# Kernel tuning notes

Hardware: AMD Instinct MI355X
Metric: run time of the kernel (lower is better)

The kernel has to match this reference:

```python
import jax, jax.numpy as jnp
import numpy as np

B = 131072
GI, GO = 4, 4          # input/output pathway groups
NI, NO = 64, 32        # neurons per input group (256/4), per output group (128/4)


def _gelu(t):
    # torch F.gelu default = exact erf gelu
    return jax.nn.gelu(t, approximate=False)


def setup_inputs() -> dict:
    key = jax.random.key(0)
    ks = jax.random.split(key, 16)
    s = 0.02
    return {
        "x":  jax.random.normal(ks[0], (B, 784), jnp.float32),
        "W1": jax.random.normal(ks[1], (512, 784), jnp.float32) * s,
        "b1": jax.random.normal(ks[2], (512,), jnp.float32) * s,
        "W2": jax.random.normal(ks[3], (256, 512), jnp.float32) * s,
        "b2": jax.random.normal(ks[4], (256,), jnp.float32) * s,
        "W3": jax.random.normal(ks[5], (128, 256), jnp.float32) * s,
        "b3": jax.random.normal(ks[6], (128,), jnp.float32) * s,
        "W4": jax.random.normal(ks[7], (64, 128), jnp.float32) * s,
        "b4": jax.random.normal(ks[8], (64,), jnp.float32) * s,
        "W5": jax.random.normal(ks[9], (32, 64), jnp.float32) * s,
        "b5": jax.random.normal(ks[10], (32,), jnp.float32) * s,
        "W6": jax.random.normal(ks[11], (10, 32), jnp.float32) * s,
        "b6": jax.random.normal(ks[12], (10,), jnp.float32) * s,
        "Wr": jax.random.normal(ks[13], (GI * GO, 256), jnp.float32) * s,
        "br": jax.random.normal(ks[14], (GI * GO,), jnp.float32) * s,
    }


def reference(x, W1, b1, W2, b2, W3, b3, W4, b4, W5, b5, W6, b6, Wr, br):
    # pre-middle dense chain (middle_layer == 3)
    h = _gelu(x @ W1.T + b1)          # [B, 512]
    mid_in = _gelu(h @ W2.T + b2)     # [B, 256]

    # router over 16 pathways; pathway_idx = i*GO + j -> reshape [B, GI, GO]
    pw = jax.nn.softmax(mid_in @ Wr.T + br, axis=-1).reshape(-1, GI, GO)

    # grouped pathway matmuls on fc3 (contiguous neuron groups -> reshape)
    xi = mid_in.reshape(-1, GI, NI)            # [B, GI, NI]
    W3g = W3.reshape(GO, NO, GI, NI)           # [GO, NO, GI, NI]
    part = jnp.einsum('bgi,ongi->bgon', xi, W3g)            # [B, GI, GO, NO]
    part = part + b3.reshape(GO, NO)[None, None]            # bias per pathway
    mid_out = jnp.einsum('bgo,bgon->bon', pw, part).reshape(-1, GO * NO)  # [B,128]
    mid_out = _gelu(mid_out)

    # post-middle dense chain
    h = _gelu(mid_out @ W4.T + b4)    # [B, 64]
    h = _gelu(h @ W5.T + b5)          # [B, 32]
    return h @ W6.T + b6              # [B, 10]
```

## Files before the change

kernel.cpp:

```cpp
#include <hip/hip_runtime.h>
#include <cstdint>

typedef _Float16 f16;
typedef _Float16 f16x4 __attribute__((ext_vector_type(4)));
typedef _Float16 f16x8 __attribute__((ext_vector_type(8)));
typedef float f32x4 __attribute__((ext_vector_type(4)));

#define MFMA16(a, b, c) __builtin_amdgcn_mfma_f32_16x16x32_f16((a), (b), (c), 0, 0, 0)
#define SBAR() __builtin_amdgcn_s_barrier()
#define SCHEDB() __builtin_amdgcn_sched_barrier(0)

__device__ __forceinline__ float gelu_f(float x) {
    const float u = x * (1.5957691216f + 0.0713548163f * x * x);
    return x * __builtin_amdgcn_rcpf(1.0f + __expf(-u));
}

__device__ __forceinline__ void load_lds16(const void* g, void* l) {
    __builtin_amdgcn_global_load_lds(
        (const __attribute__((address_space(1))) void*)(uintptr_t)g,
        (__attribute__((address_space(3))) void*)(uint32_t)(uintptr_t)l,
        16, 0, 0);
}

__global__ void k_prep(const float* __restrict__ W1, const float* __restrict__ W2,
                       const float* __restrict__ W3, const float* __restrict__ W4,
                       const float* __restrict__ W5, const float* __restrict__ W6,
                       const float* __restrict__ Wr,
                       f16* __restrict__ W1p, f16* __restrict__ W2f, f16* __restrict__ W3f,
                       f16* __restrict__ W4f, f16* __restrict__ W5f, f16* __restrict__ W6p,
                       f16* __restrict__ Wrf) {
    int i = blockIdx.x * 256 + threadIdx.x;
    if (i < 425984) {
        int r = i / 832, c = i - r * 832;
        W1p[i] = (f16)(c < 784 ? W1[r * 784 + c] : 0.0f);
        return;
    }
    i -= 425984;
    if (i < 131072) { W2f[i] = (f16)W2[i]; return; }
    i -= 131072;
    if (i < 32768) { W3f[i] = (f16)W3[i]; return; }
    i -= 32768;
    if (i < 8192) { W4f[i] = (f16)W4[i]; return; }
    i -= 8192;
    if (i < 2048) { W5f[i] = (f16)W5[i]; return; }
    i -= 2048;
    if (i < 512) {
        int r = i >> 5, c = i & 31;
        W6p[i] = (f16)(r < 10 ? W6[r * 32 + c] : 0.0f);
        return;
    }
    i -= 512;
    if (i < 4096) { Wrf[i] = (f16)Wr[i]; return; }
}

__global__ __launch_bounds__(256, 2)
void k_gemm1(const float* __restrict__ A, const f16* __restrict__ Bw,
             const float* __restrict__ bias, f16* __restrict__ C) {
    __shared__ float As[2][128 * 32];
    __shared__ f16   Bs[2][256 * 32];
    const int tid = threadIdx.x;
    const int wave = tid >> 6, lane = tid & 63;
    const int nt = blockIdx.x & 1;
    const size_t mt = blockIdx.x >> 1;
    const size_t row0 = mt * 128;
    const int col0 = nt * 256;
    const int am = lane & 15, akg = lane >> 4;
    const int wm = (wave & 1) * 64, wn = (wave >> 1) * 128;
    const f32x4 zero4 = {0.f, 0.f, 0.f, 0.f};
    f32x4 acc[4][8];
#pragma unroll
    for (int i = 0; i < 4; ++i)
#pragma unroll
        for (int j = 0; j < 8; ++j) acc[i][j] = zero4;

    const int arow_l = lane >> 3, aps = lane & 7;
    const int brow_l = lane >> 2, bps = lane & 3;

    auto stage = [&](int kt, int buf) {
        const int kb = kt * 32;
#pragma unroll
        for (int i = 0; i < 4; ++i) {
            const int inst = wave * 4 + i;
            const int row = inst * 8 + arow_l;
            const int ls = aps ^ (row & 7);
            int c = kb + ls * 4;
            if (c > 780) c = 768;
            load_lds16(A + (row0 + row) * (size_t)784 + c, &As[buf][inst * 256]);
        }
#pragma unroll
        for (int i = 0; i < 4; ++i) {
            const int inst = wave * 4 + i;
            const int row = inst * 16 + brow_l;
            const int ls = bps ^ ((row >> 1) & 3);
            load_lds16(Bw + (size_t)(col0 + row) * 832 + kb + ls * 8, &Bs[buf][inst * 512]);
        }
    };

    stage(0, 0);

    for (int kt = 0; kt < 26; ++kt) {
        const int cur = kt & 1;
        if (kt + 1 < 26) {
            stage(kt + 1, cur ^ 1);
            asm volatile("s_waitcnt vmcnt(8)" ::: "memory");
        } else {
            asm volatile("s_waitcnt vmcnt(0)" ::: "memory");
        }
        SBAR();
        SCHEDB();
        f16x8 af[4];
#pragma unroll
        for (int i = 0; i < 4; ++i) {
            const int row = wm + i * 16 + am;
            const int rx = row & 7;
            const f32x4 lo = *(const f32x4*)&As[cur][row * 32 + (((akg << 1) ^ rx) << 2)];
            const f32x4 hi = *(const f32x4*)&As[cur][row * 32 + ((((akg << 1) | 1) ^ rx) << 2)];
            f16x8 v;
            v[0] = (f16)lo[0]; v[1] = (f16)lo[1]; v[2] = (f16)lo[2]; v[3] = (f16)lo[3];
            v[4] = (f16)hi[0]; v[5] = (f16)hi[1]; v[6] = (f16)hi[2]; v[7] = (f16)hi[3];
            af[i] = v;
        }
        f16x8 bf[8];
#pragma unroll
        for (int j = 0; j < 8; ++j) {
            const int row = wn + j * 16 + am;
            bf[j] = *(const f16x8*)&Bs[cur][row * 32 + ((akg ^ ((row >> 1) & 3)) << 3)];
        }
#pragma unroll
        for (int i = 0; i < 4; ++i)
#pragma unroll
            for (int j = 0; j < 8; ++j)
                acc[i][j] = MFMA16(bf[j], af[i], acc[i][j]);
        SCHEDB();
        if (kt + 1 < 26) SBAR();
    }
    const int cc = akg * 4;
#pragma unroll
    for (int i = 0; i < 4; ++i) {
        const size_t row = row0 + wm + i * 16 + am;
#pragma unroll
        for (int j = 0; j < 8; ++j) {
            const int col = col0 + wn + j * 16 + cc;
            const float4 b4 = *(const float4*)(bias + col);
            f16x4 v;
            v[0] = (f16)gelu_f(acc[i][j][0] + b4.x);
            v[1] = (f16)gelu_f(acc[i][j][1] + b4.y);
            v[2] = (f16)gelu_f(acc[i][j][2] + b4.z);
            v[3] = (f16)gelu_f(acc[i][j][3] + b4.w);
            *(f16x4*)(C + row * 512 + col) = v;
        }
    }
}

__global__ __launch_bounds__(512, 2)
void k_mid(const f16* __restrict__ H1v, const f16* __restrict__ W2f,
           const float* __restrict__ b2,
           const f16* __restrict__ W3f, const float* __restrict__ b3,
           const f16* __restrict__ W4f, const float* __restrict__ b4,
           const f16* __restrict__ W5f, const float* __restrict__ b5,
           const f16* __restrict__ W6p, const float* __restrict__ b6v,
           const f16* __restrict__ Wrf, const float* __restrict__ brv,
           float* __restrict__ OUT) {
    __shared__ __align__(16) char smem[141312];
    f16* Am = (f16*)smem;
    f16* Bm = (f16*)(smem + 32768);
    f16* s_mid = (f16*)smem;
    float* s_pw = (float*)(smem + 67584);
    f16* s_mo = (f16*)(smem + 77824);
    f16* s_h4 = (f16*)(smem + 112640);
    f16* s_h5 = (f16*)(smem + 131072);
    const int tid = threadIdx.x, wave = tid >> 6, lane = tid & 63;
    const size_t row0 = (size_t)blockIdx.x * 128;
    const int am = lane & 15, akg = lane >> 4, ak = akg * 8;
    const int wm = (wave & 1) * 64, wn = (wave >> 1) * 64;
    const f32x4 zero4 = {0.f, 0.f, 0.f, 0.f};
    f32x4 acc[4][4];
#pragma unroll
    for (int i = 0; i < 4; ++i)
#pragma unroll
        for (int j = 0; j < 4; ++j) acc[i][j] = zero4;

    auto stage = [&](int kt, int buf) {
        const int kb = kt * 64;
#pragma unroll
        for (int t = 0; t < 2; ++t) {
            const int idx = t * 512 + tid;
            const int row = idx >> 3;
            const int ls = (idx & 7) ^ (row & 7);
            load_lds16(H1v + (row0 + row) * 512 + kb + ls * 8,
                       Am + buf * 8192 + (t * 512 + wave * 64) * 8);
        }
#pragma unroll
        for (int t = 0; t < 4; ++t) {
            const int idx = t * 512 + tid;
            const int row = idx >> 3;
            const int ls = (idx & 7) ^ (row & 7);
            load_lds16(W2f + (size_t)row * 512 + kb + ls * 8,
                       Bm + buf * 16384 + (t * 512 + wave * 64) * 8);
        }
    };

    stage(0, 0);
    for (int kt = 0; kt < 8; ++kt) {
        const int cur = kt & 1;
        if (kt + 1 < 8) {
            stage(kt + 1, cur ^ 1);
            asm volatile("s_waitcnt vmcnt(6)" ::: "memory");
        } else {
            asm volatile("s_waitcnt vmcnt(0)" ::: "memory");
        }
        SBAR();
        SCHEDB();
#pragma unroll
        for (int ks = 0; ks < 2; ++ks) {
            f16x8 af[4], bf[4];
#pragma unroll
            for (int i = 0; i < 4; ++i) {
                const int row = wm + i * 16 + am;
                af[i] = *(const f16x8*)&Am[cur * 8192 + row * 64 +
                                           ((((ks << 2) | akg) ^ (row & 7)) << 3)];
            }
#pragma unroll
            for (int j = 0; j < 4; ++j) {
                const int row = wn + j * 16 + am;
                bf[j] = *(const f16x8*)&Bm[cur * 16384 + row * 64 +
                                           ((((ks << 2) | akg) ^ (row & 7)) << 3)];
            }
#pragma unroll
            for (int i = 0; i < 4; ++i)
#pragma unroll
                for (int j = 0; j < 4; ++j)
                    acc[i][j] = MFMA16(bf[j], af[i], acc[i][j]);
        }
        SCHEDB();
        asm volatile("s_waitcnt lgkmcnt(0)" ::: "memory");
        SBAR();
    }
    {
        const int cc = akg * 4;
#pragma unroll
        for (int i = 0; i < 4; ++i) {
            const int row = wm + i * 16 + am;
#pragma unroll
            for (int j = 0; j < 4; ++j) {
                const int col = wn + j * 16 + cc;
                const float4 bb = *(const float4*)(b2 + col);
                f16x4 v;
                v[0] = (f16)gelu_f(acc[i][j][0] + bb.x);
                v[1] = (f16)gelu_f(acc[i][j][1] + bb.y);
                v[2] = (f16)gelu_f(acc[i][j][2] + bb.z);
                v[3] = (f16)gelu_f(acc[i][j][3] + bb.w);
                *(f16x4*)&s_mid[row * 264 + col] = v;
            }
        }
    }
    __syncthreads();

    const int wr = wave * 16;
    const int crow = wr + akg * 4;

    {
        f32x4 lacc = zero4;
#pragma unroll
        for (int ks = 0; ks < 8; ++ks) {
            f16x8 a = *(const f16x8*)(s_mid + (wr + am) * 264 + ks * 32 + ak);
            f16x8 b = *(const f16x8*)(Wrf + am * 256 + ks * 32 + ak);
            lacc = MFMA16(a, b, lacc);
        }
        const float brn = brv[am];
#pragma unroll
        for (int r = 0; r < 4; ++r) {
            float l = lacc[r] + brn;
            float mx = l;
#pragma unroll
            for (int m = 1; m <= 8; m <<= 1) mx = fmaxf(mx, __shfl_xor(mx, m));
            const float e = __expf(l - mx);
            float s = e;
#pragma unroll
            for (int m = 1; m <= 8; m <<= 1) s += __shfl_xor(s, m);
            const float p = e / s;
            float sg = p;
            sg += __shfl_xor(sg, 4);
            sg += __shfl_xor(sg, 8);
            s_pw[(crow + r) * 20 + am] = p;
            if (am < 4) s_pw[(crow + r) * 20 + 16 + am] = sg;
        }
    }

    {
        f16x8 a3[4][2];
#pragma unroll
        for (int g = 0; g < 4; ++g)
#pragma unroll
            for (int kh = 0; kh < 2; ++kh)
                a3[g][kh] = *(const f16x8*)(s_mid + (wr + am) * 264 + g * 64 + kh * 32 + ak);
#pragma unroll
        for (int o = 0; o < 4; ++o) {
            float pwv[4][4], sgl[4];
#pragma unroll
            for (int r = 0; r < 4; ++r) {
                sgl[r] = s_pw[(crow + r) * 20 + 16 + o];
#pragma unroll
                for (int g = 0; g < 4; ++g)
                    pwv[g][r] = s_pw[(crow + r) * 20 + g * 4 + o];
            }
#pragma unroll
            for (int ctl = 0; ctl < 2; ++ctl) {
                const int ct = o * 2 + ctl;
                const int col = ct * 16 + am;
                const float bias = b3[col];
                f32x4 oacc;
#pragma unroll
                for (int r = 0; r < 4; ++r) oacc[r] = bias * sgl[r];
#pragma unroll
                for (int g = 0; g < 4; ++g) {
                    f32x4 t = zero4;
                    t = MFMA16(a3[g][0], *(const f16x8*)(W3f + (size_t)col * 256 + g * 64 + ak), t);
                    t = MFMA16(a3[g][1], *(const f16x8*)(W3f + (size_t)col * 256 + g * 64 + 32 + ak), t);
#pragma unroll
                    for (int r = 0; r < 4; ++r) oacc[r] += pwv[g][r] * t[r];
                }
#pragma unroll
                for (int r = 0; r < 4; ++r)
                    s_mo[(crow + r) * 136 + col] = (f16)gelu_f(oacc[r]);
            }
        }
    }

    {
        f16x8 a4[4];
#pragma unroll
        for (int ks = 0; ks < 4; ++ks)
            a4[ks] = *(const f16x8*)(s_mo + (wr + am) * 136 + ks * 32 + ak);
#pragma unroll
        for (int ct = 0; ct < 4; ++ct) {
            const int col = ct * 16 + am;
            f32x4 acc4 = zero4;
#pragma unroll
            for (int ks = 0; ks < 4; ++ks)
                acc4 = MFMA16(a4[ks], *(const f16x8*)(W4f + (size_t)col * 128 + ks * 32 + ak), acc4);
            const float bias = b4[col];
#pragma unroll
            for (int r = 0; r < 4; ++r)
                s_h4[(crow + r) * 72 + col] = (f16)gelu_f(acc4[r] + bias);
        }
    }

    {
        f16x8 a5[2];
#pragma unroll
        for (int ks = 0; ks < 2; ++ks)
            a5[ks] = *(const f16x8*)(s_h4 + (wr + am) * 72 + ks * 32 + ak);
#pragma unroll
        for (int ct = 0; ct < 2; ++ct) {
            const int col = ct * 16 + am;
            f32x4 acc5 = zero4;
#pragma unroll
            for (int ks = 0; ks < 2; ++ks)
                acc5 = MFMA16(a5[ks], *(const f16x8*)(W5f + (size_t)col * 64 + ks * 32 + ak), acc5);
            const float bias = b5[col];
#pragma unroll
            for (int r = 0; r < 4; ++r)
                s_h5[(crow + r) * 40 + col] = (f16)gelu_f(acc5[r] + bias);
        }
    }

    {
        f16x8 a6 = *(const f16x8*)(s_h5 + (wr + am) * 40 + ak);
        f16x8 bw = *(const f16x8*)(W6p + am * 32 + ak);
        f32x4 acc6 = MFMA16(a6, bw, zero4);
        if (am < 10) {
            const float bb = b6v[am];
#pragma unroll
            for (int r = 0; r < 4; ++r)
                OUT[(row0 + crow + r) * 10 + am] = acc6[r] + bb;
        }
    }
}

extern "C" void kernel_launch(void* const* d_in, const int* in_sizes, int n_in,
                              void* d_out, int out_size, void* d_ws, size_t ws_size,
                              hipStream_t stream) {
    const float* x  = (const float*)d_in[0];
    const float* W1 = (const float*)d_in[1];
    const float* b1 = (const float*)d_in[2];
    const float* W2 = (const float*)d_in[3];
    const float* b2 = (const float*)d_in[4];
    const float* W3 = (const float*)d_in[5];
    const float* b3 = (const float*)d_in[6];
    const float* W4 = (const float*)d_in[7];
    const float* b4 = (const float*)d_in[8];
    const float* W5 = (const float*)d_in[9];
    const float* b5 = (const float*)d_in[10];
    const float* W6 = (const float*)d_in[11];
    const float* b6 = (const float*)d_in[12];
    const float* Wr = (const float*)d_in[13];
    const float* br = (const float*)d_in[14];
    float* out = (float*)d_out;

    const int M = in_sizes[0] / 784;

    char* ws = (char*)d_ws;
    f16* W1p = (f16*)ws; ws += 512 * 832 * 2;
    f16* W2f = (f16*)ws; ws += 256 * 512 * 2;
    f16* W3f = (f16*)ws; ws += 128 * 256 * 2;
    f16* W4f = (f16*)ws; ws += 64 * 128 * 2;
    f16* W5f = (f16*)ws; ws += 32 * 64 * 2;
    f16* W6p = (f16*)ws; ws += 16 * 32 * 2;
    f16* Wrf = (f16*)ws; ws += 16 * 256 * 2;
    f16* H1  = (f16*)ws; ws += (size_t)M * 512 * 2;

    k_prep<<<2362, 256, 0, stream>>>(W1, W2, W3, W4, W5, W6, Wr,
                                     W1p, W2f, W3f, W4f, W5f, W6p, Wrf);
    k_gemm1<<<(M / 128) * 2, 256, 0, stream>>>(x, W1p, b1, H1);
    k_mid<<<M / 128, 512, 0, stream>>>(H1, W2f, b2, W3f, b3, W4f, b4, W5f, b5,
                                       W6p, b6, Wrf, br, out);
}
```

Before: 799.6 us.

## Shrink tiles and LDS footprint to raise occupancy in both GEMM kernels

```diff
diff --git a/kernel.cpp b/kernel.cpp
--- a/kernel.cpp
+++ b/kernel.cpp
@@ -53,94 +53,95 @@
     if (i < 4096) { Wrf[i] = (f16)Wr[i]; return; }
 }
 
-__global__ __launch_bounds__(256, 2)
+__global__ __launch_bounds__(256, 4)
 void k_gemm1(const float* __restrict__ A, const f16* __restrict__ Bw,
              const float* __restrict__ bias, f16* __restrict__ C) {
-    __shared__ float As[2][128 * 32];
-    __shared__ f16   Bs[2][256 * 32];
+    __shared__ f16 Bs[2][128 * 32];
     const int tid = threadIdx.x;
     const int wave = tid >> 6, lane = tid & 63;
-    const int nt = blockIdx.x & 1;
-    const size_t mt = blockIdx.x >> 1;
-    const size_t row0 = mt * 128;
-    const int col0 = nt * 256;
-    const int am = lane & 15, akg = lane >> 4;
-    const int wm = (wave & 1) * 64, wn = (wave >> 1) * 128;
+    const int wg = (blockIdx.x & 7) * 512 + (blockIdx.x >> 3);
+    const size_t row0 = (size_t)(wg >> 2) * 128;
+    const int col0 = (wg & 3) * 128;
+    const int am = lane & 15, akg = lane >> 4, ak = akg * 8;
+    const int wm = wave * 32;
     const f32x4 zero4 = {0.f, 0.f, 0.f, 0.f};
-    f32x4 acc[4][8];
-#pragma unroll
-    for (int i = 0; i < 4; ++i)
+    f32x4 acc[2][8];
+#pragma unroll
+    for (int i = 0; i < 2; ++i)
 #pragma unroll
         for (int j = 0; j < 8; ++j) acc[i][j] = zero4;
 
-    const int arow_l = lane >> 3, aps = lane & 7;
-    const int brow_l = lane >> 2, bps = lane & 3;
-
-    auto stage = [&](int kt, int buf) {
+    auto stageB = [&](int kt, int buf) {
         const int kb = kt * 32;
 #pragma unroll
-        for (int i = 0; i < 4; ++i) {
-            const int inst = wave * 4 + i;
-            const int row = inst * 8 + arow_l;
-            const int ls = aps ^ (row & 7);
-            int c = kb + ls * 4;
-            if (c > 780) c = 768;
-            load_lds16(A + (row0 + row) * (size_t)784 + c, &As[buf][inst * 256]);
-        }
-#pragma unroll
-        for (int i = 0; i < 4; ++i) {
-            const int inst = wave * 4 + i;
-            const int row = inst * 16 + brow_l;
-            const int ls = bps ^ ((row >> 1) & 3);
-            load_lds16(Bw + (size_t)(col0 + row) * 832 + kb + ls * 8, &Bs[buf][inst * 512]);
+        for (int t = 0; t < 2; ++t) {
+            const int idx = t * 256 + tid;
+            const int row = idx >> 2;
+            const int ls = (idx & 3) ^ ((row >> 1) & 3);
+            load_lds16(Bw + (size_t)(col0 + row) * 832 + kb + ls * 8,
+                       &Bs[buf][(t * 256 + wave * 64) * 8]);
         }
     };
 
-    stage(0, 0);
-
-    for (int kt = 0; kt < 26; ++kt) {
+    stageB(0, 0);
+
+    for (int kt = 0; kt < 25; ++kt) {
         const int cur = kt & 1;
-        if (kt + 1 < 26) {
-            stage(kt + 1, cur ^ 1);
-            asm volatile("s_waitcnt vmcnt(8)" ::: "memory");
+        const int kb = kt * 32;
+        float4 ra[2][2];
+        {
+            int c = kb + ak;
+            if (c > 776) c = 768;
+#pragma unroll
+            for (int i = 0; i < 2; ++i) {
+                const float* p = A + (row0 + wm + i * 16 + am) * (size_t)784 + c;
+                ra[i][0] = *(const float4*)p;
+                ra[i][1] = *(const float4*)(p + 4);
+            }
+        }
+        SCHEDB();
+        if (kt + 1 < 25) {
+            stageB(kt + 1, cur ^ 1);
+            asm volatile("s_waitcnt vmcnt(2)" ::: "memory");
         } else {
             asm volatile("s_waitcnt vmcnt(0)" ::: "memory");
         }
         SBAR();
         SCHEDB();
-        f16x8 af[4];
-#pragma unroll
-        for (int i = 0; i < 4; ++i) {
-            const int row = wm + i * 16 + am;
-            const int rx = row & 7;
-            const f32x4 lo = *(const f32x4*)&As[cur][row * 32 + (((akg << 1) ^ rx) << 2)];
-            const f32x4 hi = *(const f32x4*)&As[cur][row * 32 + ((((akg << 1) | 1) ^ rx) << 2)];
+        f16x8 af[2];
+#pragma unroll
+        for (int i = 0; i < 2; ++i) {
             f16x8 v;
-            v[0] = (f16)lo[0]; v[1] = (f16)lo[1]; v[2] = (f16)lo[2]; v[3] = (f16)lo[3];
-            v[4] = (f16)hi[0]; v[5] = (f16)hi[1]; v[6] = (f16)hi[2]; v[7] = (f16)hi[3];
+            v[0] = (f16)ra[i][0].x; v[1] = (f16)ra[i][0].y;
+            v[2] = (f16)ra[i][0].z; v[3] = (f16)ra[i][0].w;
+            v[4] = (f16)ra[i][1].x; v[5] = (f16)ra[i][1].y;
+            v[6] = (f16)ra[i][1].z; v[7] = (f16)ra[i][1].w;
             af[i] = v;
         }
-        f16x8 bf[8];
+#pragma unroll
+        for (int jh = 0; jh < 2; ++jh) {
+            f16x8 bf[4];
+#pragma unroll
+            for (int j = 0; j < 4; ++j) {
+                const int row = jh * 64 + j * 16 + am;
+                bf[j] = *(const f16x8*)&Bs[cur][row * 32 + ((akg ^ ((row >> 1) & 3)) << 3)];
+            }
+#pragma unroll
+            for (int i = 0; i < 2; ++i)
+#pragma unroll
+                for (int j = 0; j < 4; ++j)
+                    acc[i][jh * 4 + j] = MFMA16(bf[j], af[i], acc[i][jh * 4 + j]);
+        }
+        SCHEDB();
+        SBAR();
+    }
+    const int cc = akg * 4;
+#pragma unroll
+    for (int i = 0; i < 2; ++i) {
+        const size_t row = row0 + wm + i * 16 + am;
 #pragma unroll
         for (int j = 0; j < 8; ++j) {
-            const int row = wn + j * 16 + am;
-            bf[j] = *(const f16x8*)&Bs[cur][row * 32 + ((akg ^ ((row >> 1) & 3)) << 3)];
-        }
-#pragma unroll
-        for (int i = 0; i < 4; ++i)
-#pragma unroll
-            for (int j = 0; j < 8; ++j)
-                acc[i][j] = MFMA16(bf[j], af[i], acc[i][j]);
-        SCHEDB();
-        if (kt + 1 < 26) SBAR();
-    }
-    const int cc = akg * 4;
-#pragma unroll
-    for (int i = 0; i < 4; ++i) {
-        const size_t row = row0 + wm + i * 16 + am;
-#pragma unroll
-        for (int j = 0; j < 8; ++j) {
-            const int col = col0 + wn + j * 16 + cc;
+            const int col = col0 + j * 16 + cc;
             const float4 b4 = *(const float4*)(bias + col);
             f16x4 v;
             v[0] = (f16)gelu_f(acc[i][j][0] + b4.x);
@@ -152,7 +153,7 @@
     }
 }
 
-__global__ __launch_bounds__(512, 2)
+__global__ __launch_bounds__(512, 4)
 void k_mid(const f16* __restrict__ H1v, const f16* __restrict__ W2f,
            const float* __restrict__ b2,
            const f16* __restrict__ W3f, const float* __restrict__ b3,
@@ -161,14 +162,11 @@
            const f16* __restrict__ W6p, const float* __restrict__ b6v,
            const f16* __restrict__ Wrf, const float* __restrict__ brv,
            float* __restrict__ OUT) {
-    __shared__ __align__(16) char smem[141312];
+    __shared__ __align__(16) char smem[77824];
     f16* Am = (f16*)smem;
-    f16* Bm = (f16*)(smem + 32768);
+    f16* Bm = (f16*)(smem + 16384);
     f16* s_mid = (f16*)smem;
     float* s_pw = (float*)(smem + 67584);
-    f16* s_mo = (f16*)(smem + 77824);
-    f16* s_h4 = (f16*)(smem + 112640);
-    f16* s_h5 = (f16*)(smem + 131072);
     const int tid = threadIdx.x, wave = tid >> 6, lane = tid & 63;
     const size_t row0 = (size_t)blockIdx.x * 128;
     const int am = lane & 15, akg = lane >> 4, ak = akg * 8;
@@ -181,50 +179,47 @@
         for (int j = 0; j < 4; ++j) acc[i][j] = zero4;
 
     auto stage = [&](int kt, int buf) {
-        const int kb = kt * 64;
+        const int kb = kt * 32;
+        {
+            const int row = tid >> 2;
+            const int ls = (tid & 3) ^ ((row >> 1) & 3);
+            load_lds16(H1v + (row0 + row) * 512 + kb + ls * 8,
+                       Am + buf * 4096 + wave * 512);
+        }
 #pragma unroll
         for (int t = 0; t < 2; ++t) {
             const int idx = t * 512 + tid;
-            const int row = idx >> 3;
-            const int ls = (idx & 7) ^ (row & 7);
-            load_lds16(H1v + (row0 + row) * 512 + kb + ls * 8,
-                       Am + buf * 8192 + (t * 512 + wave * 64) * 8);
-        }
-#pragma unroll
-        for (int t = 0; t < 4; ++t) {
-            const int idx = t * 512 + tid;
-            const int row = idx >> 3;
-            const int ls = (idx & 7) ^ (row & 7);
+            const int row = idx >> 2;
+            const int ls = (idx & 3) ^ ((row >> 1) & 3);
             load_lds16(W2f + (size_t)row * 512 + kb + ls * 8,
-                       Bm + buf * 16384 + (t * 512 + wave * 64) * 8);
+                       Bm + buf * 8192 + t * 4096 + wave * 512);
         }
     };
 
     stage(0, 0);
-    for (int kt = 0; kt < 8; ++kt) {
+    for (int kt = 0; kt < 16; ++kt) {
         const int cur = kt & 1;
-        if (kt + 1 < 8) {
+        if (kt + 1 < 16) {
             stage(kt + 1, cur ^ 1);
-            asm volatile("s_waitcnt vmcnt(6)" ::: "memory");
+            asm volatile("s_waitcnt vmcnt(3)" ::: "memory");
         } else {
             asm volatile("s_waitcnt vmcnt(0)" ::: "memory");
         }
         SBAR();
         SCHEDB();
-#pragma unroll
-        for (int ks = 0; ks < 2; ++ks) {
+        {
             f16x8 af[4], bf[4];
 #pragma unroll
             for (int i = 0; i < 4; ++i) {
                 const int row = wm + i * 16 + am;
-                af[i] = *(const f16x8*)&Am[cur * 8192 + row * 64 +
-                                           ((((ks << 2) | akg) ^ (row & 7)) << 3)];
+                af[i] = *(const f16x8*)&Am[cur * 4096 + row * 32 +
+                                           ((akg ^ ((row >> 1) & 3)) << 3)];
             }
 #pragma unroll
             for (int j = 0; j < 4; ++j) {
                 const int row = wn + j * 16 + am;
-                bf[j] = *(const f16x8*)&Bm[cur * 16384 + row * 64 +
-                                           ((((ks << 2) | akg) ^ (row & 7)) << 3)];
+                bf[j] = *(const f16x8*)&Bm[cur * 8192 + row * 32 +
+                                           ((akg ^ ((row >> 1) & 3)) << 3)];
             }
 #pragma unroll
             for (int i = 0; i < 4; ++i)
@@ -258,12 +253,13 @@
 
     const int wr = wave * 16;
     const int crow = wr + akg * 4;
+    f16* wslice = s_mid + wr * 264;
 
     {
         f32x4 lacc = zero4;
 #pragma unroll
         for (int ks = 0; ks < 8; ++ks) {
-            f16x8 a = *(const f16x8*)(s_mid + (wr + am) * 264 + ks * 32 + ak);
+            f16x8 a = *(const f16x8*)(wslice + am * 264 + ks * 32 + ak);
             f16x8 b = *(const f16x8*)(Wrf + am * 256 + ks * 32 + ak);
             lacc = MFMA16(a, b, lacc);
         }
@@ -293,7 +289,9 @@
         for (int g = 0; g < 4; ++g)
 #pragma unroll
             for (int kh = 0; kh < 2; ++kh)
-                a3[g][kh] = *(const f16x8*)(s_mid + (wr + am) * 264 + g * 64 + kh * 32 + ak);
+                a3[g][kh] = *(const f16x8*)(wslice + am * 264 + g * 64 + kh * 32 + ak);
+        asm volatile("s_waitcnt lgkmcnt(0)" ::: "memory");
+        SCHEDB();
 #pragma unroll
         for (int o = 0; o < 4; ++o) {
             float pwv[4][4], sgl[4];
@@ -322,7 +320,7 @@
                 }
 #pragma unroll
                 for (int r = 0; r < 4; ++r)
-                    s_mo[(crow + r) * 136 + col] = (f16)gelu_f(oacc[r]);
+                    wslice[(akg * 4 + r) * 136 + col] = (f16)gelu_f(oacc[r]);
             }
         }
     }
@@ -331,7 +329,7 @@
         f16x8 a4[4];
 #pragma unroll
         for (int ks = 0; ks < 4; ++ks)
-            a4[ks] = *(const f16x8*)(s_mo + (wr + am) * 136 + ks * 32 + ak);
+            a4[ks] = *(const f16x8*)(wslice + am * 136 + ks * 32 + ak);
 #pragma unroll
         for (int ct = 0; ct < 4; ++ct) {
             const int col = ct * 16 + am;
@@ -342,7 +340,7 @@
             const float bias = b4[col];
 #pragma unroll
             for (int r = 0; r < 4; ++r)
-                s_h4[(crow + r) * 72 + col] = (f16)gelu_f(acc4[r] + bias);
+                wslice[2176 + (akg * 4 + r) * 72 + col] = (f16)gelu_f(acc4[r] + bias);
         }
     }
 
@@ -350,7 +348,7 @@
         f16x8 a5[2];
 #pragma unroll
         for (int ks = 0; ks < 2; ++ks)
-            a5[ks] = *(const f16x8*)(s_h4 + (wr + am) * 72 + ks * 32 + ak);
+            a5[ks] = *(const f16x8*)(wslice + 2176 + am * 72 + ks * 32 + ak);
 #pragma unroll
         for (int ct = 0; ct < 2; ++ct) {
             const int col = ct * 16 + am;
@@ -361,12 +359,12 @@
             const float bias = b5[col];
 #pragma unroll
             for (int r = 0; r < 4; ++r)
-                s_h5[(crow + r) * 40 + col] = (f16)gelu_f(acc5[r] + bias);
-        }
-    }
-
-    {
-        f16x8 a6 = *(const f16x8*)(s_h5 + (wr + am) * 40 + ak);
+                wslice[3328 + (akg * 4 + r) * 40 + col] = (f16)gelu_f(acc5[r] + bias);
+        }
+    }
+
+    {
+        f16x8 a6 = *(const f16x8*)(wslice + 3328 + am * 40 + ak);
         f16x8 bw = *(const f16x8*)(W6p + am * 32 + ak);
         f32x4 acc6 = MFMA16(a6, bw, zero4);
         if (am < 10) {
@@ -412,7 +410,7 @@
 
     k_prep<<<2362, 256, 0, stream>>>(W1, W2, W3, W4, W5, W6, Wr,
                                      W1p, W2f, W3f, W4f, W5f, W6p, Wrf);
-    k_gemm1<<<(M / 128) * 2, 256, 0, stream>>>(x, W1p, b1, H1);
+    k_gemm1<<<(M / 128) * 4, 256, 0, stream>>>(x, W1p, b1, H1);
     k_mid<<<M / 128, 512, 0, stream>>>(H1, W2f, b2, W3f, b3, W4f, b4, W5f, b5,
                                        W6p, b6, Wrf, br, out);
 }
```

Result: slower. 1.049 ms (+31.2%).
